# Performance work log

Measured on AMD Instinct MI355X. Metric: run time of the kernel, lower is better.

Reference implementation:

```python
import jax, jax.numpy as jnp
import numpy as np

_ENTROPY_EPS = 1e-9
TOP_K = 2

def setup_inputs() -> dict:
    key = jax.random.key(0)
    k1, k2, k3, k4 = jax.random.split(key, 4)
    B, S, D, E, F = 4, 1024, 1024, 8, 4096
    hidden = jax.random.normal(k1, (B, S, D), dtype=jnp.float32)
    route_weights = jax.random.uniform(k2, (B, S, E), dtype=jnp.float32)
    # expert FFN params, scaled like standard init
    w1 = jax.random.normal(k3, (E, D, F), dtype=jnp.float32) * (1.0 / np.sqrt(D))
    b1 = jnp.zeros((E, F), dtype=jnp.float32)
    w2 = jax.random.normal(k4, (E, F, D), dtype=jnp.float32) * (1.0 / np.sqrt(F))
    b2 = jnp.zeros((E, D), dtype=jnp.float32)
    return {"hidden": hidden, "route_weights": route_weights,
            "w1": w1, "b1": b1, "w2": w2, "b2": b2}

def reference(hidden, route_weights, w1, b1, w2, b2):
    # --- compile (SPARSE_TOP_K): top-k gating + renormalization ---
    E = route_weights.shape[-1]
    top_w, top_i = jax.lax.top_k(route_weights, TOP_K)          # [B,S,k]
    denom = jnp.maximum(jnp.sum(top_w, axis=-1, keepdims=True), _ENTROPY_EPS)
    sel_w = top_w / denom                                        # [B,S,k]
    # combine weights per expert: combine[b,s,e] = sum_k sel_w * 1[top_i==e]
    onehot = jax.nn.one_hot(top_i, E, dtype=hidden.dtype)        # [B,S,k,E]
    combine = jnp.sum(sel_w[..., None] * onehot, axis=-2)        # [B,S,E]
    # --- dispatch: expert FFN on all tokens, masked-combine ---
    # (same math as gather/scatter token-packed dispatch: out = sum_k w_k * expert_{i_k}(x))
    h = jax.nn.gelu(jnp.einsum('bsd,edf->bsef', hidden, w1) + b1)  # [B,S,E,F]
    y = jnp.einsum('bsef,efd->bsed', h, w2) + b2                   # [B,S,E,D]
    out = jnp.einsum('bsed,bse->bsd', y, combine)                  # [B,S,D]
    return out
```

## Files before the change

kernel.cpp:

```cpp
#include <hip/hip_runtime.h>


#define E_ 8
#define D_ 1024
#define F_ 4096
#define NTOK 4096
#define NPAIR 8192
#define CAP 2048

typedef short bf16x8 __attribute__((ext_vector_type(8)));
typedef float f32x4 __attribute__((ext_vector_type(4)));

#define GLOBAL_AS __attribute__((address_space(1)))
#define LDS_AS __attribute__((address_space(3)))

__device__ __forceinline__ ushort f2bf(float f) {
  unsigned u = __builtin_bit_cast(unsigned, f);
  unsigned r = (u + 0x7FFFu + ((u >> 16) & 1u)) >> 16;
  return (ushort)r;
}

__global__ void gate_kernel(const float* __restrict__ rw, int* __restrict__ counts,
                            int* __restrict__ tok_list, float* __restrict__ w_list) {
  int t = blockIdx.x * 256 + threadIdx.x;
  if (t >= NTOK) return;
  float v[E_];
#pragma unroll
  for (int e = 0; e < E_; ++e) v[e] = rw[t * E_ + e];
  int i0 = 0;
  float m0 = v[0];
#pragma unroll
  for (int e = 1; e < E_; ++e)
    if (v[e] > m0) { m0 = v[e]; i0 = e; }
  int i1 = -1;
  float m1 = -1e30f;
#pragma unroll
  for (int e = 0; e < E_; ++e)
    if (e != i0 && v[e] > m1) { m1 = v[e]; i1 = e; }
  float denom = fmaxf(m0 + m1, 1e-9f);
  float w0 = m0 / denom, w1 = m1 / denom;
  int p0 = atomicAdd(&counts[i0], 1);
  if (p0 < CAP) { tok_list[i0 * CAP + p0] = t; w_list[i0 * CAP + p0] = w0; }
  int p1 = atomicAdd(&counts[i1], 1);
  if (p1 < CAP) { tok_list[i1 * CAP + p1] = t; w_list[i1 * CAP + p1] = w1; }
}

__global__ void scan_kernel(const int* __restrict__ counts, int* __restrict__ offsets) {
  if (threadIdx.x == 0) {
    int a = 0;
    for (int e = 0; e < E_; ++e) {
      offsets[e] = a;
      int c = counts[e];
      if (c > CAP) c = CAP;
      a += c;
    }
    offsets[E_] = a;
  }
}

__global__ __launch_bounds__(256) void gather_kernel(
    const float* __restrict__ hidden, const int* __restrict__ counts,
    const int* __restrict__ offsets, const int* __restrict__ tok_list,
    const float* __restrict__ w_list, ushort* __restrict__ Xg,
    int* __restrict__ tok_pack, float* __restrict__ w_pack) {
  int bid = blockIdx.x;
  int e = bid >> 11;
  int pos = bid & (CAP - 1);
  int cnt = counts[e];
  if (cnt > CAP) cnt = CAP;
  if (pos >= cnt) return;
  int row = offsets[e] + pos;
  int t = tok_list[e * CAP + pos];
  if (threadIdx.x == 0) {
    tok_pack[row] = t;
    w_pack[row] = w_list[e * CAP + pos];
  }
  float4 v = *(const float4*)(hidden + (size_t)t * D_ + threadIdx.x * 4);
  ushort4 o;
  o.x = f2bf(v.x); o.y = f2bf(v.y); o.z = f2bf(v.z); o.w = f2bf(v.w);
  *(ushort4*)(Xg + (size_t)row * D_ + threadIdx.x * 4) = o;
}

__global__ __launch_bounds__(256) void transpose_bf16(const float* __restrict__ src,
                                                      ushort* __restrict__ dst, int R, int C) {
  __shared__ ushort t[64][65];
  int e = blockIdx.z;
  int r0 = blockIdx.y * 64, c0 = blockIdx.x * 64;
  const float* s = src + (size_t)e * R * C;
  int tr = threadIdx.x >> 4;
  int tc = (threadIdx.x & 15) * 4;
#pragma unroll
  for (int i = 0; i < 4; ++i) {
    int r = tr + i * 16;
    float4 v = *(const float4*)(s + (size_t)(r0 + r) * C + c0 + tc);
    t[r][tc + 0] = f2bf(v.x);
    t[r][tc + 1] = f2bf(v.y);
    t[r][tc + 2] = f2bf(v.z);
    t[r][tc + 3] = f2bf(v.w);
  }
  __syncthreads();
  ushort* d = dst + (size_t)e * C * R;
#pragma unroll
  for (int i = 0; i < 4; ++i) {
    int oc = tr + i * 16;
    ushort4 o;
    o.x = t[tc + 0][oc];
    o.y = t[tc + 1][oc];
    o.z = t[tc + 2][oc];
    o.w = t[tc + 3][oc];
    *(ushort4*)(d + (size_t)(c0 + oc) * R + r0 + tc) = o;
  }
}

template <int PASS>
__global__ __launch_bounds__(256) void gemm_kernel(
    const ushort* __restrict__ A, const ushort* __restrict__ B,
    const int* __restrict__ offsets, const int* __restrict__ tok_pack,
    const float* __restrict__ w_pack, const float* __restrict__ bias,
    void* __restrict__ outp, int K, int N) {
  __shared__ ushort As[128 * 32];
  __shared__ ushort Bs[128 * 32];
  const int e = blockIdx.z;
  const int rb = blockIdx.y;
  const int cb = blockIdx.x;
  const int seg_lo = offsets[e], seg_hi = offsets[e + 1];
  if (rb * 128 >= seg_hi - seg_lo) return;
  const int row0 = seg_lo + rb * 128;
  const int tid = threadIdx.x;
  const int l = tid & 63, w = tid >> 6;
  const int wr = w >> 1, wc = w & 1;

  f32x4 acc[4][4] = {};

  const ushort* Be = B + (size_t)e * N * K;
  const int colbase = cb * 128;
  const int arow_l = (l >> 2);
  const int acol_l = (l & 3) * 8;

  for (int kt = 0; kt < K; kt += 32) {
#pragma unroll
    for (int i = 0; i < 2; ++i) {
      int c = w + i * 4;
      int r = c * 16 + arow_l;
      int grA = row0 + r;
      if (grA > NPAIR - 1) grA = NPAIR - 1;
      const ushort* gpA = A + (size_t)grA * K + kt + acol_l;
      __builtin_amdgcn_global_load_lds((const GLOBAL_AS void*)gpA,
                                       (LDS_AS void*)(As + c * 512), 16, 0, 0);
      int grB = colbase + r;
      const ushort* gpB = Be + (size_t)grB * K + kt + acol_l;
      __builtin_amdgcn_global_load_lds((const GLOBAL_AS void*)gpB,
                                       (LDS_AS void*)(Bs + c * 512), 16, 0, 0);
    }
    __syncthreads();
    bf16x8 af[4], bf[4];
#pragma unroll
    for (int m = 0; m < 4; ++m)
      af[m] = *(const bf16x8*)(As + (wr * 64 + m * 16 + (l & 15)) * 32 + (l >> 4) * 8);
#pragma unroll
    for (int n = 0; n < 4; ++n)
      bf[n] = *(const bf16x8*)(Bs + (wc * 64 + n * 16 + (l & 15)) * 32 + (l >> 4) * 8);
#pragma unroll
    for (int m = 0; m < 4; ++m)
#pragma unroll
      for (int n = 0; n < 4; ++n)
        acc[m][n] = __builtin_amdgcn_mfma_f32_16x16x32_bf16(af[m], bf[n], acc[m][n], 0, 0, 0);
    __syncthreads();
  }

#pragma unroll
  for (int m = 0; m < 4; ++m) {
#pragma unroll
    for (int n = 0; n < 4; ++n) {
      int col = colbase + wc * 64 + n * 16 + (l & 15);
      float bv = bias[e * N + col];
#pragma unroll
      for (int reg = 0; reg < 4; ++reg) {
        int row = row0 + wr * 64 + m * 16 + (l >> 4) * 4 + reg;
        if (row < seg_hi) {
          if constexpr (PASS == 0) {
            float x = acc[m][n][reg] + bv;
            float x3 = x * x * x;
            float th = tanhf(0.7978845608028654f * (x + 0.044715f * x3));
            float g = 0.5f * x * (1.0f + th);
            ((ushort*)outp)[(size_t)row * N + col] = f2bf(g);
          } else {
            float val = w_pack[row] * (acc[m][n][reg] + bv);
            atomicAdd(&((float*)outp)[(size_t)tok_pack[row] * D_ + col], val);
          }
        }
      }
    }
  }
}

extern "C" void kernel_launch(void* const* d_in, const int* in_sizes, int n_in,
                              void* d_out, int out_size, void* d_ws, size_t ws_size,
                              hipStream_t stream) {
  const float* hidden = (const float*)d_in[0];
  const float* route = (const float*)d_in[1];
  const float* w1 = (const float*)d_in[2];
  const float* b1 = (const float*)d_in[3];
  const float* w2 = (const float*)d_in[4];
  const float* b2 = (const float*)d_in[5];
  float* out = (float*)d_out;

  char* ws = (char*)d_ws;
  int* counts = (int*)ws;
  int* offsets = (int*)(ws + 64);
  int* tok_list = (int*)(ws + 4096);
  float* w_list = (float*)(ws + 4096 + 65536);
  int* tok_pack = (int*)(ws + 4096 + 2 * 65536);
  float* w_pack = (float*)(ws + 4096 + 2 * 65536 + 32768);
  ushort* Xg = (ushort*)(ws + 262144);
  ushort* H = (ushort*)(ws + 262144 + (size_t)16 * 1024 * 1024);
  ushort* W1t = (ushort*)(ws + 262144 + (size_t)80 * 1024 * 1024);
  ushort* W2t = (ushort*)(ws + 262144 + (size_t)144 * 1024 * 1024);

  hipMemsetAsync(counts, 0, 64, stream);
  hipMemsetAsync(d_out, 0, (size_t)out_size * sizeof(float), stream);

  transpose_bf16<<<dim3(F_ / 64, D_ / 64, E_), 256, 0, stream>>>(w1, W1t, D_, F_);
  transpose_bf16<<<dim3(D_ / 64, F_ / 64, E_), 256, 0, stream>>>(w2, W2t, F_, D_);

  gate_kernel<<<NTOK / 256, 256, 0, stream>>>(route, counts, tok_list, w_list);
  scan_kernel<<<1, 64, 0, stream>>>(counts, offsets);
  gather_kernel<<<E_ * CAP, 256, 0, stream>>>(hidden, counts, offsets, tok_list,
                                              w_list, Xg, tok_pack, w_pack);

  gemm_kernel<0><<<dim3(F_ / 128, CAP / 128, E_), 256, 0, stream>>>(
      Xg, W1t, offsets, tok_pack, w_pack, b1, H, D_, F_);
  gemm_kernel<1><<<dim3(D_ / 128, CAP / 128, E_), 256, 0, stream>>>(
      H, W2t, offsets, tok_pack, w_pack, b2, out, F_, D_);
}
```

Before: 704.3 us.

## Double-buffer LDS tiles in expert GEMM and swap grid row/column order

The GEMM kernel now uses two LDS buffers, so the global-to-LDS load for the next K tile is issued before the MFMA work on the current tile, hiding load latency behind compute. Precomputed base pointers replace per-iteration address math, and the loop has one barrier per iteration instead of two. The grid is also reordered so row blocks vary fastest, which changes which blocks share weight tiles in cache and lets idle row blocks exit in clusters. LDS use doubles, which may lower occupancy.

```diff
diff --git a/kernel.cpp b/kernel.cpp
--- a/kernel.cpp
+++ b/kernel.cpp
@@ -118,11 +118,11 @@
     const int* __restrict__ offsets, const int* __restrict__ tok_pack,
     const float* __restrict__ w_pack, const float* __restrict__ bias,
     void* __restrict__ outp, int K, int N) {
-  __shared__ ushort As[128 * 32];
-  __shared__ ushort Bs[128 * 32];
+  __shared__ ushort As[2][128 * 32];
+  __shared__ ushort Bs[2][128 * 32];
   const int e = blockIdx.z;
-  const int rb = blockIdx.y;
-  const int cb = blockIdx.x;
+  const int rb = blockIdx.x;
+  const int cb = blockIdx.y;
   const int seg_lo = offsets[e], seg_hi = offsets[e + 1];
   if (rb * 128 >= seg_hi - seg_lo) return;
   const int row0 = seg_lo + rb * 128;
@@ -137,36 +137,60 @@
   const int arow_l = (l >> 2);
   const int acol_l = (l & 3) * 8;
 
-  for (int kt = 0; kt < K; kt += 32) {
-#pragma unroll
-    for (int i = 0; i < 2; ++i) {
-      int c = w + i * 4;
-      int r = c * 16 + arow_l;
-      int grA = row0 + r;
-      if (grA > NPAIR - 1) grA = NPAIR - 1;
-      const ushort* gpA = A + (size_t)grA * K + kt + acol_l;
-      __builtin_amdgcn_global_load_lds((const GLOBAL_AS void*)gpA,
-                                       (LDS_AS void*)(As + c * 512), 16, 0, 0);
-      int grB = colbase + r;
-      const ushort* gpB = Be + (size_t)grB * K + kt + acol_l;
-      __builtin_amdgcn_global_load_lds((const GLOBAL_AS void*)gpB,
-                                       (LDS_AS void*)(Bs + c * 512), 16, 0, 0);
-    }
-    __syncthreads();
-    bf16x8 af[4], bf[4];
+  const int c0 = w, c1 = w + 4;
+  int rA0 = row0 + c0 * 16 + arow_l;
+  int rA1 = row0 + c1 * 16 + arow_l;
+  if (rA0 > NPAIR - 1) rA0 = NPAIR - 1;
+  if (rA1 > NPAIR - 1) rA1 = NPAIR - 1;
+  const ushort* pA0 = A + (size_t)rA0 * K + acol_l;
+  const ushort* pA1 = A + (size_t)rA1 * K + acol_l;
+  const ushort* pB0 = Be + (size_t)(colbase + c0 * 16 + arow_l) * K + acol_l;
+  const ushort* pB1 = Be + (size_t)(colbase + c1 * 16 + arow_l) * K + acol_l;
+
+#define STAGE(buf, kt)                                                              \
+  do {                                                                              \
+    __builtin_amdgcn_global_load_lds((const GLOBAL_AS void*)(pA0 + (kt)),           \
+                                     (LDS_AS void*)(As[buf] + c0 * 512), 16, 0, 0); \
+    __builtin_amdgcn_global_load_lds((const GLOBAL_AS void*)(pA1 + (kt)),           \
+                                     (LDS_AS void*)(As[buf] + c1 * 512), 16, 0, 0); \
+    __builtin_amdgcn_global_load_lds((const GLOBAL_AS void*)(pB0 + (kt)),           \
+                                     (LDS_AS void*)(Bs[buf] + c0 * 512), 16, 0, 0); \
+    __builtin_amdgcn_global_load_lds((const GLOBAL_AS void*)(pB1 + (kt)),           \
+                                     (LDS_AS void*)(Bs[buf] + c1 * 512), 16, 0, 0); \
+  } while (0)
+
+  const int nk = K / 32;
+  STAGE(0, 0);
+  asm volatile("s_waitcnt vmcnt(0)" ::: "memory");
+  __builtin_amdgcn_s_barrier();
+  __builtin_amdgcn_sched_barrier(0);
+
+  int cur = 0;
+  for (int t = 0; t < nk; ++t) {
+    if (t + 1 < nk) STAGE(cur ^ 1, (t + 1) * 32);
+
+    const ushort* as = As[cur];
+    const ushort* bs = Bs[cur];
+    bf16x8 af[4], bfr[4];
 #pragma unroll
     for (int m = 0; m < 4; ++m)
-      af[m] = *(const bf16x8*)(As + (wr * 64 + m * 16 + (l & 15)) * 32 + (l >> 4) * 8);
+      af[m] = *(const bf16x8*)(as + (wr * 64 + m * 16 + (l & 15)) * 32 + (l >> 4) * 8);
 #pragma unroll
     for (int n = 0; n < 4; ++n)
-      bf[n] = *(const bf16x8*)(Bs + (wc * 64 + n * 16 + (l & 15)) * 32 + (l >> 4) * 8);
+      bfr[n] = *(const bf16x8*)(bs + (wc * 64 + n * 16 + (l & 15)) * 32 + (l >> 4) * 8);
 #pragma unroll
     for (int m = 0; m < 4; ++m)
 #pragma unroll
       for (int n = 0; n < 4; ++n)
-        acc[m][n] = __builtin_amdgcn_mfma_f32_16x16x32_bf16(af[m], bf[n], acc[m][n], 0, 0, 0);
-    __syncthreads();
-  }
+        acc[m][n] = __builtin_amdgcn_mfma_f32_16x16x32_bf16(af[m], bfr[n], acc[m][n], 0, 0, 0);
+
+    __builtin_amdgcn_sched_barrier(0);
+    asm volatile("s_waitcnt vmcnt(0)" ::: "memory");
+    __builtin_amdgcn_s_barrier();
+    __builtin_amdgcn_sched_barrier(0);
+    cur ^= 1;
+  }
+#undef STAGE
 
 #pragma unroll
   for (int m = 0; m < 4; ++m) {
@@ -228,8 +252,8 @@
   gather_kernel<<<E_ * CAP, 256, 0, stream>>>(hidden, counts, offsets, tok_list,
                                               w_list, Xg, tok_pack, w_pack);
 
-  gemm_kernel<0><<<dim3(F_ / 128, CAP / 128, E_), 256, 0, stream>>>(
+  gemm_kernel<0><<<dim3(CAP / 128, F_ / 128, E_), 256, 0, stream>>>(
       Xg, W1t, offsets, tok_pack, w_pack, b1, H, D_, F_);
-  gemm_kernel<1><<<dim3(D_ / 128, CAP / 128, E_), 256, 0, stream>>>(
+  gemm_kernel<1><<<dim3(CAP / 128, D_ / 128, E_), 256, 0, stream>>>(
       H, W2t, offsets, tok_pack, w_pack, b2, out, F_, D_);
 }
```

Result: slower. 923.0 us (+31.0%).
